# Kernel tuning notes

Measured on AMD Instinct MI355X. Metric: run time of the kernel, lower is better.

The kernel has to match this reference:

```python
import jax, jax.numpy as jnp
import numpy as np

N_PATCHES = 256
PATCH = 16
D = 768
H = 12
DH = D // H
L = 12
OUT_D = 10
EPS = 1e-5


def _pos_embed(seq_len, d):
    i = np.arange(seq_len)[:, None].astype(np.float64)
    j = np.arange(d)[None, :].astype(np.float64)
    angle_even = i / 10000 ** (j / d)
    angle_odd = i / 10000 ** ((j - 1) / d)
    pe = np.where(np.arange(d)[None, :] % 2 == 0, np.sin(angle_even), np.cos(angle_odd))
    return jnp.asarray(pe, dtype=jnp.float32)


def _layernorm(x, g, b):
    mu = jnp.mean(x, axis=-1, keepdims=True)
    var = jnp.var(x, axis=-1, keepdims=True)
    return (x - mu) * jax.lax.rsqrt(var + EPS) * g + b


def setup_inputs() -> dict:
    key = jax.random.key(0)
    ks = jax.random.split(key, 16)
    s = 0.02
    return {
        "images": jax.random.normal(ks[0], (64, 1, N_PATCHES * PATCH), dtype=jnp.float32),
        "Wemb": jax.random.normal(ks[1], (D, PATCH), dtype=jnp.float32) * s,
        "bemb": jnp.zeros((D,), jnp.float32),
        "cls": jax.random.uniform(ks[2], (1, D), dtype=jnp.float32),
        "Wq": jax.random.normal(ks[3], (L, H, DH, DH), dtype=jnp.float32) * s,
        "bq": jnp.zeros((L, H, DH), jnp.float32),
        "Wk": jax.random.normal(ks[4], (L, H, DH, DH), dtype=jnp.float32) * s,
        "bk": jnp.zeros((L, H, DH), jnp.float32),
        "Wv": jax.random.normal(ks[5], (L, H, DH, DH), dtype=jnp.float32) * s,
        "bv": jnp.zeros((L, H, DH), jnp.float32),
        "ln1_g": jnp.ones((L, D), jnp.float32),
        "ln1_b": jnp.zeros((L, D), jnp.float32),
        "ln2_g": jnp.ones((L, D), jnp.float32),
        "ln2_b": jnp.zeros((L, D), jnp.float32),
        "W1": jax.random.normal(ks[6], (L, 4 * D, D), dtype=jnp.float32) * s,
        "b1": jnp.zeros((L, 4 * D), jnp.float32),
        "W2": jax.random.normal(ks[7], (L, D, 4 * D), dtype=jnp.float32) * s,
        "b2": jnp.zeros((L, D), jnp.float32),
        "Whead": jax.random.normal(ks[8], (OUT_D, D), dtype=jnp.float32) * s,
        "bhead": jnp.zeros((OUT_D,), jnp.float32),
    }


def reference(images, Wemb, bemb, cls, Wq, bq, Wk, bk, Wv, bv,
              ln1_g, ln1_b, ln2_g, ln2_b, W1, b1, W2, b2, Whead, bhead):
    n = images.shape[0]
    # patchify: (N,1,Lspec) -> (N, n_patches, patch_size)
    patches = images.reshape(n, N_PATCHES, PATCH)
    tok = jnp.einsum("npi,di->npd", patches, Wemb) + bemb  # linear embed
    tok = jnp.concatenate([jnp.broadcast_to(cls[None], (n, 1, D)), tok], axis=1)
    tok = tok + _pos_embed(N_PATCHES + 1, D)[None]  # (N, S, D), S = 257

    scale = 1.0 / jnp.sqrt(jnp.float32(DH))
    for l in range(L):
        x = tok
        h = _layernorm(x, ln1_g[l], ln1_b[l]).reshape(n, -1, H, DH)
        q = jnp.einsum("nshd,hod->nsho", h, Wq[l]) + bq[l][None, None]
        k = jnp.einsum("nshd,hod->nsho", h, Wk[l]) + bk[l][None, None]
        v = jnp.einsum("nshd,hod->nsho", h, Wv[l]) + bv[l][None, None]
        att = jax.nn.softmax(jnp.einsum("nqho,nkho->nhqk", q, k) * scale, axis=-1)
        o = jnp.einsum("nhqk,nkho->nqho", att, v).reshape(n, -1, D)
        x = x + o  # residual (no output projection in original MSA)
        h2 = _layernorm(x, ln2_g[l], ln2_b[l])
        mlp = jax.nn.gelu(jnp.einsum("nsd,fd->nsf", h2, W1[l]) + b1[l], approximate=False)
        tok = x + jnp.einsum("nsf,df->nsd", mlp, W2[l]) + b2[l]

    logits = tok[:, 0] @ Whead.T + bhead
    return jax.nn.softmax(logits, axis=-1)
```

## Files before the change

### kernel.cpp

```cpp
#include <hip/hip_runtime.h>
#include <math.h>
#include <stdint.h>

#define N_IMG 64
#define S_LEN 257
#define D_MODEL 768
#define H_HEADS 12
#define L_LAYERS 12
#define F_HID 3072
#define OUT_DIM 10
#define R_ROWS (N_IMG * S_LEN)
#define R_PAD 16512
#define SKV 320

typedef unsigned short ushort_t;
typedef __attribute__((ext_vector_type(4))) float f32x4;
typedef __attribute__((ext_vector_type(8))) short short8;
typedef __attribute__((ext_vector_type(2))) unsigned int u32x2;

__device__ __forceinline__ ushort_t f2bf(float x) {
    unsigned u = __float_as_uint(x);
    u += 0x7fffu + ((u >> 16) & 1u);
    return (ushort_t)(u >> 16);
}
__device__ __forceinline__ unsigned pack2(float a, float b) {
    return (unsigned)f2bf(a) | ((unsigned)f2bf(b) << 16);
}

__device__ __forceinline__ void glds16(const ushort_t* g, const ushort_t* l) {
    __builtin_amdgcn_global_load_lds(
        (const __attribute__((address_space(1))) unsigned int*)(uintptr_t)g,
        (__attribute__((address_space(3))) unsigned int*)(uintptr_t)l,
        16, 0, 0);
}

__global__ __launch_bounds__(256) void pos_kernel(float* __restrict__ pos) {
    int i = blockIdx.x;
    int t = threadIdx.x;
    for (int u = 0; u < 3; ++u) {
        int j = t + 256 * u;
        double e = (double)(j & ~1) / 768.0;
        double angle = (double)i * exp(-e * 9.210340371976184);
        double v = (j & 1) ? cos(angle) : sin(angle);
        pos[i * 768 + j] = (float)v;
    }
}

__global__ __launch_bounds__(256) void embed_kernel(const float* __restrict__ images,
                                                    const float* __restrict__ Wemb,
                                                    const float* __restrict__ bemb,
                                                    const float* __restrict__ cls,
                                                    const float* __restrict__ pos,
                                                    float* __restrict__ tok) {
    int b = blockIdx.x;
    int n = b / S_LEN, s = b % S_LEN;
    int t = threadIdx.x;
    __shared__ float p[16];
    if (s > 0 && t < 16) p[t] = images[n * 4096 + (s - 1) * 16 + t];
    __syncthreads();
    for (int u = 0; u < 3; ++u) {
        int d = t + 256 * u;
        float acc;
        if (s == 0) {
            acc = cls[d];
        } else {
            acc = bemb[d];
            const float4* w = (const float4*)(Wemb + d * 16);
            float4 w0 = w[0], w1 = w[1], w2 = w[2], w3 = w[3];
            acc += p[0] * w0.x + p[1] * w0.y + p[2] * w0.z + p[3] * w0.w;
            acc += p[4] * w1.x + p[5] * w1.y + p[6] * w1.z + p[7] * w1.w;
            acc += p[8] * w2.x + p[9] * w2.y + p[10] * w2.z + p[11] * w2.w;
            acc += p[12] * w3.x + p[13] * w3.y + p[14] * w3.z + p[15] * w3.w;
        }
        tok[(size_t)b * 768 + d] = acc + pos[s * 768 + d];
    }
}

__global__ __launch_bounds__(256) void ln_kernel(const float* __restrict__ x,
                                                 const float* __restrict__ g,
                                                 const float* __restrict__ b,
                                                 ushort_t* __restrict__ y) {
    int row = blockIdx.x * 4 + (threadIdx.x >> 6);
    int lane = threadIdx.x & 63;
    const float* xr = x + (size_t)row * 768 + lane * 4;
    float4 a0 = *(const float4*)xr;
    float4 a1 = *(const float4*)(xr + 256);
    float4 a2 = *(const float4*)(xr + 512);
    float s = (a0.x + a0.y + a0.z + a0.w) + (a1.x + a1.y + a1.z + a1.w) + (a2.x + a2.y + a2.z + a2.w);
    float sq = a0.x*a0.x + a0.y*a0.y + a0.z*a0.z + a0.w*a0.w
             + a1.x*a1.x + a1.y*a1.y + a1.z*a1.z + a1.w*a1.w
             + a2.x*a2.x + a2.y*a2.y + a2.z*a2.z + a2.w*a2.w;
    for (int o = 32; o; o >>= 1) {
        s += __shfl_xor(s, o);
        sq += __shfl_xor(sq, o);
    }
    float mu = s * (1.0f / 768.0f);
    float var = sq * (1.0f / 768.0f) - mu * mu;
    float rs = rsqrtf(var + 1e-5f);
    ushort_t* yr = y + (size_t)row * 768 + lane * 4;
#pragma unroll
    for (int i = 0; i < 3; ++i) {
        float4 av = (i == 0) ? a0 : (i == 1) ? a1 : a2;
        const float4 gg = *(const float4*)(g + lane * 4 + i * 256);
        const float4 bb = *(const float4*)(b + lane * 4 + i * 256);
        float o0 = (av.x - mu) * rs * gg.x + bb.x;
        float o1 = (av.y - mu) * rs * gg.y + bb.y;
        float o2 = (av.z - mu) * rs * gg.z + bb.z;
        float o3 = (av.w - mu) * rs * gg.w + bb.w;
        *(u32x2*)(yr + i * 256) = (u32x2){pack2(o0, o1), pack2(o2, o3)};
    }
}

__global__ __launch_bounds__(256) void conv_layer(const float* __restrict__ Wq,
                                                  const float* __restrict__ Wk,
                                                  const float* __restrict__ Wv,
                                                  const float* __restrict__ W1l,
                                                  const float* __restrict__ W2l,
                                                  ushort_t* __restrict__ wqkvbf,
                                                  ushort_t* __restrict__ w1bf,
                                                  ushort_t* __restrict__ w2bf) {
    const int NQKV = H_HEADS * 192 * 64;
    const int NW = F_HID * D_MODEL;
    int idx = (blockIdx.x * 256 + threadIdx.x) * 4;
    if (idx < NQKV) {
        int h = idx / (192 * 64);
        int rem = idx - h * 192 * 64;
        int o3 = rem >> 6, d = rem & 63;
        const float* src;
        int o;
        if (o3 < 64)       { src = Wq; o = o3; }
        else if (o3 < 128) { src = Wk; o = o3 - 64; }
        else               { src = Wv; o = o3 - 128; }
        float4 v = *(const float4*)(src + ((size_t)(h * 64 + o)) * 64 + d);
        *(u32x2*)(wqkvbf + idx) = (u32x2){pack2(v.x, v.y), pack2(v.z, v.w)};
    } else if (idx < NQKV + NW) {
        int i = idx - NQKV;
        float4 v = *(const float4*)(W1l + i);
        *(u32x2*)(w1bf + i) = (u32x2){pack2(v.x, v.y), pack2(v.z, v.w)};
    } else {
        int i = idx - NQKV - NW;
        float4 v = *(const float4*)(W2l + i);
        *(u32x2*)(w2bf + i) = (u32x2){pack2(v.x, v.y), pack2(v.z, v.w)};
    }
}

__global__ __launch_bounds__(256) void qkv_mfma(const ushort_t* __restrict__ xbf,
                                                const ushort_t* __restrict__ wqkv,
                                                const float* __restrict__ bq,
                                                const float* __restrict__ bk,
                                                const float* __restrict__ bv,
                                                ushort_t* __restrict__ qhb,
                                                ushort_t* __restrict__ khb,
                                                ushort_t* __restrict__ vtb) {
    __shared__ ushort_t As[128 * 64];
    int rt = blockIdx.x;
    int h = blockIdx.y;
    int t = threadIdx.x, lane = t & 63, wid = t >> 6;
    int wr = wid >> 1, wc = wid & 1;
    {
        int lr = t >> 3, lg = t & 7;
#pragma unroll
        for (int u = 0; u < 4; ++u) {
            int r = u * 32 + lr;
            int grow = rt * 128 + r;
            if (grow >= R_ROWS) grow = R_ROWS - 1;
            short8 a = *(const short8*)(xbf + (size_t)grow * 768 + h * 64 + lg * 8);
            *(short8*)&As[r * 64 + (lg ^ (r & 7)) * 8] = a;
        }
    }
    __syncthreads();
    int frow = lane & 15, g = lane >> 4;
    const ushort_t* wb = wqkv + (size_t)h * (192 * 64);
    f32x4 acc[4][6];
#pragma unroll
    for (int m = 0; m < 4; ++m)
#pragma unroll
        for (int n = 0; n < 6; ++n) acc[m][n] = (f32x4){0.f, 0.f, 0.f, 0.f};
#pragma unroll
    for (int kk = 0; kk < 2; ++kk) {
        short8 af[4], bfr[6];
#pragma unroll
        for (int m = 0; m < 4; ++m) {
            int r = wr * 64 + m * 16 + frow;
            af[m] = *(const short8*)&As[r * 64 + ((kk * 4 + g) ^ (r & 7)) * 8];
        }
#pragma unroll
        for (int n = 0; n < 6; ++n)
            bfr[n] = *(const short8*)(wb + (size_t)(wc * 96 + n * 16 + frow) * 64 + kk * 32 + g * 8);
#pragma unroll
        for (int m = 0; m < 4; ++m)
#pragma unroll
            for (int n = 0; n < 6; ++n)
                acc[m][n] = __builtin_amdgcn_mfma_f32_16x16x32_bf16(bfr[n], af[m], acc[m][n], 0, 0, 0);
    }
#pragma unroll
    for (int m = 0; m < 4; ++m) {
        int token = rt * 128 + wr * 64 + m * 16 + frow;
        if (token < R_ROWS) {
            unsigned nimg = (unsigned)token / 257u;
            unsigned s = (unsigned)token - nimg * 257u;
            size_t qk_base = ((size_t)(nimg * H_HEADS + h) * 257 + s) * 64;
            size_t v_base = (size_t)(nimg * H_HEADS + h) * (64 * SKV);
#pragma unroll
            for (int n = 0; n < 6; ++n) {
                int c = wc * 96 + n * 16 + g * 4;
                f32x4 a = acc[m][n];
                if (c < 64) {
                    const float4 bb = *(const float4*)(bq + h * 64 + c);
                    *(u32x2*)(qhb + qk_base + c) = (u32x2){
                        pack2((a[0] + bb.x) * 0.125f, (a[1] + bb.y) * 0.125f),
                        pack2((a[2] + bb.z) * 0.125f, (a[3] + bb.w) * 0.125f)};
                } else if (c < 128) {
                    const float4 bb = *(const float4*)(bk + h * 64 + (c - 64));
                    *(u32x2*)(khb + qk_base + (c - 64)) = (u32x2){
                        pack2(a[0] + bb.x, a[1] + bb.y), pack2(a[2] + bb.z, a[3] + bb.w)};
                } else {
                    const float4 bb = *(const float4*)(bv + h * 64 + (c - 128));
                    vtb[v_base + (size_t)(c - 128 + 0) * SKV + s] = f2bf(a[0] + bb.x);
                    vtb[v_base + (size_t)(c - 128 + 1) * SKV + s] = f2bf(a[1] + bb.y);
                    vtb[v_base + (size_t)(c - 128 + 2) * SKV + s] = f2bf(a[2] + bb.z);
                    vtb[v_base + (size_t)(c - 128 + 3) * SKV + s] = f2bf(a[3] + bb.w);
                }
            }
        }
    }
}

template <int NST>
__global__ __launch_bounds__(256) void attn_mfma(const ushort_t* __restrict__ qh,
                                                 const ushort_t* __restrict__ kh,
                                                 const ushort_t* __restrict__ vT,
                                                 float* __restrict__ tok, int base) {
    __shared__ ushort_t Plds[4][NST][1024];
    int nh = blockIdx.x;
    int h = nh % H_HEADS, n = nh / H_HEADS;
    int t = threadIdx.x, w = t >> 6, lane = t & 63;
    int lq = lane & 15, g = lane >> 4;
    const size_t hoff = ((size_t)n * H_HEADS + h) * (S_LEN * 64);
    const ushort_t* qhp = qh + hoff;
    const ushort_t* khp = kh + hoff;
    const ushort_t* vp  = vT + ((size_t)n * H_HEADS + h) * (64 * SKV);
    const int xorm = (lq & 7) << 4;

    short8 qf[NST][2];
    int qr0[NST];
    float m[NST], lsum[NST];
    f32x4 o[NST][4];
#pragma unroll
    for (int s = 0; s < NST; ++s) {
        int qrow = base + s * 64 + w * 16 + lq;
        qr0[s] = qrow;
        int qcl = qrow > 256 ? 256 : qrow;
#pragma unroll
        for (int kk = 0; kk < 2; ++kk)
            qf[s][kk] = *(const short8*)(qhp + (size_t)qcl * 64 + kk * 32 + g * 8);
        m[s] = -INFINITY; lsum[s] = 0.f;
#pragma unroll
        for (int dt = 0; dt < 4; ++dt) o[s][dt] = (f32x4){0.f, 0.f, 0.f, 0.f};
    }

    for (int kt = 0; kt < 5; ++kt) {
        short8 ah[4][2];
#pragma unroll
        for (int st = 0; st < 4; ++st) {
            int key = kt * 64 + st * 16 + lq;
            int kcl = key > 256 ? 256 : key;
            const ushort_t* krh = khp + (size_t)kcl * 64 + g * 8;
            ah[st][0] = *(const short8*)krh;
            ah[st][1] = *(const short8*)(krh + 32);
        }
        f32x4 c[NST][4];
#pragma unroll
        for (int s = 0; s < NST; ++s)
#pragma unroll
            for (int st = 0; st < 4; ++st) {
                c[s][st] = (f32x4){0.f, 0.f, 0.f, 0.f};
#pragma unroll
                for (int kk = 0; kk < 2; ++kk)
                    c[s][st] = __builtin_amdgcn_mfma_f32_16x16x32_bf16(ah[st][kk], qf[s][kk], c[s][st], 0, 0, 0);
            }
        float scale[NST];
        unsigned pw[NST][4][2];
#pragma unroll
        for (int s = 0; s < NST; ++s) {
            float tmax = -INFINITY;
#pragma unroll
            for (int st = 0; st < 4; ++st)
#pragma unroll
                for (int j = 0; j < 4; ++j) {
                    int key = kt * 64 + st * 16 + g * 4 + j;
                    float sv = (key <= 256) ? c[s][st][j] : -INFINITY;
                    c[s][st][j] = sv;
                    tmax = fmaxf(tmax, sv);
                }
            tmax = fmaxf(tmax, __shfl_xor(tmax, 16));
            tmax = fmaxf(tmax, __shfl_xor(tmax, 32));
            float mn = fmaxf(m[s], tmax);
            scale[s] = __expf(m[s] - mn);
            float psum = 0.f;
#pragma unroll
            for (int st = 0; st < 4; ++st) {
                float p0 = __expf(c[s][st][0] - mn), p1 = __expf(c[s][st][1] - mn);
                float p2 = __expf(c[s][st][2] - mn), p3 = __expf(c[s][st][3] - mn);
                psum += (p0 + p1) + (p2 + p3);
                pw[s][st][0] = pack2(p0, p1);
                pw[s][st][1] = pack2(p2, p3);
            }
            psum += __shfl_xor(psum, 16);
            psum += __shfl_xor(psum, 32);
            lsum[s] = lsum[s] * scale[s] + psum;
            m[s] = mn;
        }
#pragma unroll
        for (int s = 0; s < NST; ++s) {
            char* pwave = (char*)&Plds[w][s][0];
#pragma unroll
            for (int st = 0; st < 4; ++st) {
                int off = (lq * 128 + st * 32 + g * 8) ^ xorm;
                *(u32x2*)(pwave + off) = (u32x2){pw[s][st][0], pw[s][st][1]};
            }
#pragma unroll
            for (int dt = 0; dt < 4; ++dt) {
                o[s][dt][0] *= scale[s]; o[s][dt][1] *= scale[s];
                o[s][dt][2] *= scale[s]; o[s][dt][3] *= scale[s];
            }
        }
#pragma unroll
        for (int kk = 0; kk < 2; ++kk) {
            short8 pf[NST];
#pragma unroll
            for (int s = 0; s < NST; ++s) {
                int roff = (lq * 128 + kk * 64 + g * 16) ^ xorm;
                pf[s] = *(const short8*)((char*)&Plds[w][s][0] + roff);
            }
#pragma unroll
            for (int dt = 0; dt < 4; ++dt) {
                short8 vf = *(const short8*)(vp + (size_t)(dt * 16 + lq) * SKV + kt * 64 + kk * 32 + g * 8);
#pragma unroll
                for (int s = 0; s < NST; ++s)
                    o[s][dt] = __builtin_amdgcn_mfma_f32_16x16x32_bf16(vf, pf[s], o[s][dt], 0, 0, 0);
            }
        }
    }
#pragma unroll
    for (int s = 0; s < NST; ++s) {
        if (qr0[s] < S_LEN) {
            float inv = 1.0f / lsum[s];
            float* trow = tok + ((size_t)n * S_LEN + qr0[s]) * 768 + h * 64 + g * 4;
#pragma unroll
            for (int dt = 0; dt < 4; ++dt) {
                float4 old = *(const float4*)(trow + dt * 16);
                old.x += o[s][dt][0] * inv;
                old.y += o[s][dt][1] * inv;
                old.z += o[s][dt][2] * inv;
                old.w += o[s][dt][3] * inv;
                *(float4*)(trow + dt * 16) = old;
            }
        }
    }
}

__device__ __forceinline__ float gelu_fast(float x) {
    float s = fabsf(x) * 0.70710678118654752f;
    float t = 1.0f / (1.0f + 0.3275911f * s);
    float y = t * (0.254829592f + t * (-0.284496736f + t * (1.421413741f +
              t * (-1.453152027f + t * 1.061405429f))));
    float erfa = 1.0f - y * __expf(-s * s);
    float erfv = copysignf(erfa, x);
    return 0.5f * x * (1.0f + erfv);
}

template <int MODE>
__global__ __launch_bounds__(256) void mfma_gemm(const ushort_t* __restrict__ A,
                                                 const ushort_t* __restrict__ B,
                                                 const float* __restrict__ bias,
                                                 void* __restrict__ Cv,
                                                 int K, int lda, int ldb, int ldc, int nbn) {
    __shared__ ushort_t As[2][128 * 64];
    __shared__ ushort_t Bs[2][128 * 64];
    int nwg = gridDim.x;
    int orig = blockIdx.x;
    int xcd = orig & 7, idx = orig >> 3;
    int q8 = nwg >> 3, r8 = nwg & 7;
    int cbase = (xcd < r8) ? xcd * (q8 + 1) : r8 * (q8 + 1) + (xcd - r8) * q8;
    int swz = cbase + idx;
    int bm = swz / nbn, bn = swz - bm * nbn;

    int t = threadIdx.x;
    int lane = t & 63, wid = t >> 6;
    int wr = wid >> 1, wc = wid & 1;
    const ushort_t* Ag = A + (size_t)(bm * 128) * lda;
    const ushort_t* Bg = B + (size_t)(bn * 128) * ldb;
    int srow = t >> 3;
    int swzo = ((t & 7) ^ (srow & 7)) * 8;
    int wbase = (t & 192) * 8;
    int frow = lane & 15, g = lane >> 4;
    f32x4 acc[4][4];
#pragma unroll
    for (int m = 0; m < 4; ++m)
#pragma unroll
        for (int n = 0; n < 4; ++n) acc[m][n] = (f32x4){0.f, 0.f, 0.f, 0.f};

    auto STAGE = [&](int buf, int k0) {
#pragma unroll
        for (int u = 0; u < 4; ++u) {
            glds16(Ag + (size_t)(u * 32 + srow) * lda + k0 + swzo, &As[buf][u * 2048 + wbase]);
            glds16(Bg + (size_t)(u * 32 + srow) * ldb + k0 + swzo, &Bs[buf][u * 2048 + wbase]);
        }
    };
    STAGE(0, 0);
    asm volatile("s_waitcnt vmcnt(0)" ::: "memory");
    __builtin_amdgcn_s_barrier();
    int nt = K >> 6;
    int cur = 0;
    for (int it = 0; it < nt; ++it) {
        if (it + 1 < nt) STAGE(cur ^ 1, (it + 1) * 64);
        const ushort_t* Ab = &As[cur][0];
        const ushort_t* Bb = &Bs[cur][0];
#pragma unroll
        for (int kk = 0; kk < 2; ++kk) {
            short8 af[4], bfr[4];
#pragma unroll
            for (int mi = 0; mi < 4; ++mi) {
                int r = wr * 64 + mi * 16 + frow;
                af[mi] = *(const short8*)&Ab[r * 64 + ((kk * 4 + g) ^ (r & 7)) * 8];
            }
#pragma unroll
            for (int ni = 0; ni < 4; ++ni) {
                int r = wc * 64 + ni * 16 + frow;
                bfr[ni] = *(const short8*)&Bb[r * 64 + ((kk * 4 + g) ^ (r & 7)) * 8];
            }
#pragma unroll
            for (int mi = 0; mi < 4; ++mi)
#pragma unroll
                for (int ni = 0; ni < 4; ++ni)
                    acc[mi][ni] = __builtin_amdgcn_mfma_f32_16x16x32_bf16(bfr[ni], af[mi], acc[mi][ni], 0, 0, 0);
        }
        if (it + 1 < nt) {
            asm volatile("s_waitcnt vmcnt(0) lgkmcnt(0)" ::: "memory");
            __builtin_amdgcn_s_barrier();
            cur ^= 1;
        }
    }
    int row0 = bm * 128 + wr * 64 + frow;
    int col0 = bn * 128 + wc * 64 + g * 4;
#pragma unroll
    for (int n = 0; n < 4; ++n) {
        int col = col0 + n * 16;
        float4 bb = {0.f, 0.f, 0.f, 0.f};
        if (bias) bb = *(const float4*)(bias + col);
#pragma unroll
        for (int mi = 0; mi < 4; ++mi) {
            int row = row0 + mi * 16;
            f32x4 a = acc[mi][n];
            float v0 = a[0] + bb.x, v1 = a[1] + bb.y, v2 = a[2] + bb.z, v3 = a[3] + bb.w;
            if (MODE == 0) {
                v0 = gelu_fast(v0); v1 = gelu_fast(v1); v2 = gelu_fast(v2); v3 = gelu_fast(v3);
                *(u32x2*)((ushort_t*)Cv + (size_t)row * ldc + col) =
                    (u32x2){pack2(v0, v1), pack2(v2, v3)};
            } else {
                float* cp = (float*)Cv + (size_t)row * ldc + col;
                float4 old = *(const float4*)cp;
                old.x += v0; old.y += v1; old.z += v2; old.w += v3;
                *(float4*)cp = old;
            }
        }
    }
}

__global__ __launch_bounds__(64) void head_kernel(const float* __restrict__ tok,
                                                  const float* __restrict__ Whead,
                                                  const float* __restrict__ bhead,
                                                  float* __restrict__ out) {
    int n = blockIdx.x;
    int t = threadIdx.x;
    __shared__ float logits[OUT_DIM];
    if (t < OUT_DIM) {
        float acc = bhead[t];
        const float* xr = tok + (size_t)n * S_LEN * 768;
        const float* w = Whead + t * 768;
        for (int d = 0; d < 768; ++d) acc += xr[d] * w[d];
        logits[t] = acc;
    }
    __syncthreads();
    if (t == 0) {
        float m = -INFINITY;
        for (int o = 0; o < OUT_DIM; ++o) m = fmaxf(m, logits[o]);
        float ssum = 0.f;
        float e[OUT_DIM];
        for (int o = 0; o < OUT_DIM; ++o) { e[o] = expf(logits[o] - m); ssum += e[o]; }
        float inv = 1.0f / ssum;
        for (int o = 0; o < OUT_DIM; ++o) out[n * OUT_DIM + o] = e[o] * inv;
    }
}

extern "C" void kernel_launch(void* const* d_in, const int* in_sizes, int n_in,
                              void* d_out, int out_size, void* d_ws, size_t ws_size,
                              hipStream_t stream) {
    const float* images = (const float*)d_in[0];
    const float* Wemb   = (const float*)d_in[1];
    const float* bemb   = (const float*)d_in[2];
    const float* cls    = (const float*)d_in[3];
    const float* Wq     = (const float*)d_in[4];
    const float* bq     = (const float*)d_in[5];
    const float* Wk     = (const float*)d_in[6];
    const float* bk     = (const float*)d_in[7];
    const float* Wv     = (const float*)d_in[8];
    const float* bv     = (const float*)d_in[9];
    const float* ln1_g  = (const float*)d_in[10];
    const float* ln1_b  = (const float*)d_in[11];
    const float* ln2_g  = (const float*)d_in[12];
    const float* ln2_b  = (const float*)d_in[13];
    const float* W1     = (const float*)d_in[14];
    const float* b1     = (const float*)d_in[15];
    const float* W2     = (const float*)d_in[16];
    const float* b2     = (const float*)d_in[17];
    const float* Whead  = (const float*)d_in[18];
    const float* bhead  = (const float*)d_in[19];
    float* out = (float*)d_out;

    const size_t TOKP = (size_t)R_PAD * D_MODEL;
    const size_t QKSZ = (size_t)N_IMG * H_HEADS * S_LEN * 64;
    const size_t VTSZ = (size_t)N_IMG * H_HEADS * 64 * SKV;
    const size_t WSZ  = (size_t)F_HID * D_MODEL;
    float* ws   = (float*)d_ws;
    float* pos  = ws;
    float* tok  = pos + 197376;
    ushort_t* xbf  = (ushort_t*)(tok + TOKP);
    ushort_t* qhb  = xbf + TOKP;
    ushort_t* khb  = qhb + QKSZ;
    ushort_t* vtb  = khb + QKSZ;
    ushort_t* wqkvbf = vtb + VTSZ;
    ushort_t* w1bf = wqkvbf + H_HEADS * 192 * 64;
    ushort_t* w2bf = w1bf + WSZ;
    ushort_t* hid_full = w2bf + WSZ;

    const size_t hid_bytes = (size_t)R_PAD * F_HID * 2;
    const size_t needed = ((char*)hid_full - (char*)d_ws) + hid_bytes;
    int nchunk = (ws_size >= needed) ? 1 : 2;
    int FC = F_HID / nchunk;
    ushort_t* hid = (nchunk == 1) ? hid_full : qhb;

    pos_kernel<<<S_LEN, 256, 0, stream>>>(pos);
    embed_kernel<<<R_ROWS, 256, 0, stream>>>(images, Wemb, bemb, cls, pos, tok);

    for (int l = 0; l < L_LAYERS; ++l) {
        const size_t wqkv_off = (size_t)l * H_HEADS * 64 * 64;
        const size_t bqkv_off = (size_t)l * H_HEADS * 64;
        ln_kernel<<<R_ROWS / 4, 256, 0, stream>>>(tok, ln1_g + l * 768, ln1_b + l * 768, xbf);
        conv_layer<<<4752, 256, 0, stream>>>(
            Wq + wqkv_off, Wk + wqkv_off, Wv + wqkv_off,
            W1 + (size_t)l * WSZ, W2 + (size_t)l * WSZ,
            wqkvbf, w1bf, w2bf);
        qkv_mfma<<<dim3(R_PAD / 128, H_HEADS), 256, 0, stream>>>(
            xbf, wqkvbf, bq + bqkv_off, bk + bqkv_off, bv + bqkv_off, qhb, khb, vtb);
        attn_mfma<2><<<N_IMG * H_HEADS, 256, 0, stream>>>(qhb, khb, vtb, tok, 0);
        attn_mfma<3><<<N_IMG * H_HEADS, 256, 0, stream>>>(qhb, khb, vtb, tok, 128);
        ln_kernel<<<R_ROWS / 4, 256, 0, stream>>>(tok, ln2_g + l * 768, ln2_b + l * 768, xbf);
        for (int c = 0; c < nchunk; ++c) {
            int c0 = c * FC;
            mfma_gemm<0><<<(FC / 128) * (R_PAD / 128), 256, 0, stream>>>(
                xbf, w1bf + (size_t)c0 * D_MODEL, b1 + (size_t)l * F_HID + c0, hid,
                768, 768, 768, FC, FC / 128);
            mfma_gemm<1><<<(D_MODEL / 128) * (R_PAD / 128), 256, 0, stream>>>(
                hid, w2bf + c0, (c == 0) ? (b2 + (size_t)l * D_MODEL) : (const float*)nullptr,
                tok, FC, FC, F_HID, D_MODEL, D_MODEL / 128);
        }
    }
    head_kernel<<<N_IMG, 64, 0, stream>>>(tok, Whead, bhead, out);
}
```

Measured before the change: 4.823 ms.

## Enlarge MLP GEMM tiles to 256x256 with 512 threads and 4-stage LDS pipeline

Rewrites the MLP GEMM kernel to use 256x256 output tiles across 8 waves, with a K-step of 32 and a four-buffer global-to-LDS prefetch ring driven by vmcnt-based waits. Row padding grows so row counts divide by 256, and the QKV launch keeps its old grid size. The larger tiles are meant to raise arithmetic intensity and hide load latency better. In exchange, register pressure rises (32 accumulator tiles per wave), the grid has fewer blocks, which may leave CUs idle (the W2 GEMM gets only 3 column tiles), and there is extra padded work.

```diff
diff --git a/kernel.cpp b/kernel.cpp
--- a/kernel.cpp
+++ b/kernel.cpp
@@ -10,7 +10,7 @@
 #define F_HID 3072
 #define OUT_DIM 10
 #define R_ROWS (N_IMG * S_LEN)
-#define R_PAD 16512
+#define R_PAD 16640
 #define SKV 320
 
 typedef unsigned short ushort_t;
@@ -371,13 +371,13 @@
 }
 
 template <int MODE>
-__global__ __launch_bounds__(256) void mfma_gemm(const ushort_t* __restrict__ A,
-                                                 const ushort_t* __restrict__ B,
-                                                 const float* __restrict__ bias,
-                                                 void* __restrict__ Cv,
-                                                 int K, int lda, int ldb, int ldc, int nbn) {
-    __shared__ ushort_t As[2][128 * 64];
-    __shared__ ushort_t Bs[2][128 * 64];
+__global__ __launch_bounds__(512, 2) void mfma_gemm(const ushort_t* __restrict__ A,
+                                                    const ushort_t* __restrict__ B,
+                                                    const float* __restrict__ bias,
+                                                    void* __restrict__ Cv,
+                                                    int K, int lda, int ldb, int ldc, int nbn) {
+    __shared__ ushort_t As[4][256 * 32];
+    __shared__ ushort_t Bs[4][256 * 32];
     int nwg = gridDim.x;
     int orig = blockIdx.x;
     int xcd = orig & 7, idx = orig >> 3;
@@ -387,72 +387,71 @@
     int bm = swz / nbn, bn = swz - bm * nbn;
 
     int t = threadIdx.x;
-    int lane = t & 63, wid = t >> 6;
-    int wr = wid >> 1, wc = wid & 1;
-    const ushort_t* Ag = A + (size_t)(bm * 128) * lda;
-    const ushort_t* Bg = B + (size_t)(bn * 128) * ldb;
-    int srow = t >> 3;
-    int swzo = ((t & 7) ^ (srow & 7)) * 8;
-    int wbase = (t & 192) * 8;
+    int lane = t & 63, w = t >> 6;
+    int wr = w >> 2, wc = w & 3;
+    const ushort_t* Ag = A + (size_t)(bm * 256) * lda;
+    const ushort_t* Bg = B + (size_t)(bn * 256) * ldb;
     int frow = lane & 15, g = lane >> 4;
-    f32x4 acc[4][4];
-#pragma unroll
-    for (int m = 0; m < 4; ++m)
+    int srow = lane >> 2;
+    int scol = ((lane & 3) ^ ((lane >> 3) & 3)) * 8;
+    int rslot = (frow >> 1) & 3;
+
+    f32x4 acc[8][4];
+#pragma unroll
+    for (int m = 0; m < 8; ++m)
 #pragma unroll
         for (int n = 0; n < 4; ++n) acc[m][n] = (f32x4){0.f, 0.f, 0.f, 0.f};
 
-    auto STAGE = [&](int buf, int k0) {
-#pragma unroll
-        for (int u = 0; u < 4; ++u) {
-            glds16(Ag + (size_t)(u * 32 + srow) * lda + k0 + swzo, &As[buf][u * 2048 + wbase]);
-            glds16(Bg + (size_t)(u * 32 + srow) * ldb + k0 + swzo, &Bs[buf][u * 2048 + wbase]);
+    auto STAGE = [&](int buf, int kt) {
+        int k0 = kt * 32;
+#pragma unroll
+        for (int i = 0; i < 2; ++i) {
+            int rbase = w * 32 + i * 16;
+            glds16(Ag + (size_t)(rbase + srow) * lda + k0 + scol, &As[buf][rbase * 32]);
+            glds16(Bg + (size_t)(rbase + srow) * ldb + k0 + scol, &Bs[buf][rbase * 32]);
         }
     };
     STAGE(0, 0);
-    asm volatile("s_waitcnt vmcnt(0)" ::: "memory");
-    __builtin_amdgcn_s_barrier();
-    int nt = K >> 6;
-    int cur = 0;
+    STAGE(1, 1);
+    STAGE(2, 2);
+    int nt = K >> 5;
     for (int it = 0; it < nt; ++it) {
-        if (it + 1 < nt) STAGE(cur ^ 1, (it + 1) * 64);
-        const ushort_t* Ab = &As[cur][0];
-        const ushort_t* Bb = &Bs[cur][0];
-#pragma unroll
-        for (int kk = 0; kk < 2; ++kk) {
-            short8 af[4], bfr[4];
-#pragma unroll
-            for (int mi = 0; mi < 4; ++mi) {
-                int r = wr * 64 + mi * 16 + frow;
-                af[mi] = *(const short8*)&Ab[r * 64 + ((kk * 4 + g) ^ (r & 7)) * 8];
-            }
-#pragma unroll
-            for (int ni = 0; ni < 4; ++ni) {
-                int r = wc * 64 + ni * 16 + frow;
-                bfr[ni] = *(const short8*)&Bb[r * 64 + ((kk * 4 + g) ^ (r & 7)) * 8];
-            }
-#pragma unroll
-            for (int mi = 0; mi < 4; ++mi)
-#pragma unroll
-                for (int ni = 0; ni < 4; ++ni)
-                    acc[mi][ni] = __builtin_amdgcn_mfma_f32_16x16x32_bf16(bfr[ni], af[mi], acc[mi][ni], 0, 0, 0);
-        }
-        if (it + 1 < nt) {
-            asm volatile("s_waitcnt vmcnt(0) lgkmcnt(0)" ::: "memory");
-            __builtin_amdgcn_s_barrier();
-            cur ^= 1;
-        }
-    }
-    int row0 = bm * 128 + wr * 64 + frow;
-    int col0 = bn * 128 + wc * 64 + g * 4;
+        int ahead = nt - 1 - it;
+        if (ahead >= 2)      asm volatile("s_waitcnt vmcnt(8)" ::: "memory");
+        else if (ahead == 1) asm volatile("s_waitcnt vmcnt(4)" ::: "memory");
+        else                 asm volatile("s_waitcnt vmcnt(0)" ::: "memory");
+        asm volatile("s_barrier" ::: "memory");
+        if (it + 3 < nt) STAGE((it + 3) & 3, it + 3);
+        const ushort_t* Ab = &As[it & 3][0];
+        const ushort_t* Bb = &Bs[it & 3][0];
+        short8 af[8], bf[4];
+#pragma unroll
+        for (int m = 0; m < 8; ++m) {
+            int r = wr * 128 + m * 16 + frow;
+            af[m] = *(const short8*)&Ab[r * 32 + ((g ^ rslot) * 8)];
+        }
+#pragma unroll
+        for (int n = 0; n < 4; ++n) {
+            int r = wc * 64 + n * 16 + frow;
+            bf[n] = *(const short8*)&Bb[r * 32 + ((g ^ rslot) * 8)];
+        }
+#pragma unroll
+        for (int m = 0; m < 8; ++m)
+#pragma unroll
+            for (int n = 0; n < 4; ++n)
+                acc[m][n] = __builtin_amdgcn_mfma_f32_16x16x32_bf16(bf[n], af[m], acc[m][n], 0, 0, 0);
+    }
+    int row0 = bm * 256 + wr * 128 + frow;
+    int col0 = bn * 256 + wc * 64 + g * 4;
 #pragma unroll
     for (int n = 0; n < 4; ++n) {
         int col = col0 + n * 16;
         float4 bb = {0.f, 0.f, 0.f, 0.f};
         if (bias) bb = *(const float4*)(bias + col);
 #pragma unroll
-        for (int mi = 0; mi < 4; ++mi) {
-            int row = row0 + mi * 16;
-            f32x4 a = acc[mi][n];
+        for (int m = 0; m < 8; ++m) {
+            int row = row0 + m * 16;
+            f32x4 a = acc[m][n];
             float v0 = a[0] + bb.x, v1 = a[1] + bb.y, v2 = a[2] + bb.z, v3 = a[3] + bb.w;
             if (MODE == 0) {
                 v0 = gelu_fast(v0); v1 = gelu_fast(v1); v2 = gelu_fast(v2); v3 = gelu_fast(v3);
@@ -552,19 +551,19 @@
             Wq + wqkv_off, Wk + wqkv_off, Wv + wqkv_off,
             W1 + (size_t)l * WSZ, W2 + (size_t)l * WSZ,
             wqkvbf, w1bf, w2bf);
-        qkv_mfma<<<dim3(R_PAD / 128, H_HEADS), 256, 0, stream>>>(
+        qkv_mfma<<<dim3(16512 / 128, H_HEADS), 256, 0, stream>>>(
             xbf, wqkvbf, bq + bqkv_off, bk + bqkv_off, bv + bqkv_off, qhb, khb, vtb);
         attn_mfma<2><<<N_IMG * H_HEADS, 256, 0, stream>>>(qhb, khb, vtb, tok, 0);
         attn_mfma<3><<<N_IMG * H_HEADS, 256, 0, stream>>>(qhb, khb, vtb, tok, 128);
         ln_kernel<<<R_ROWS / 4, 256, 0, stream>>>(tok, ln2_g + l * 768, ln2_b + l * 768, xbf);
         for (int c = 0; c < nchunk; ++c) {
             int c0 = c * FC;
-            mfma_gemm<0><<<(FC / 128) * (R_PAD / 128), 256, 0, stream>>>(
+            mfma_gemm<0><<<(FC / 256) * (R_PAD / 256), 512, 0, stream>>>(
                 xbf, w1bf + (size_t)c0 * D_MODEL, b1 + (size_t)l * F_HID + c0, hid,
-                768, 768, 768, FC, FC / 128);
-            mfma_gemm<1><<<(D_MODEL / 128) * (R_PAD / 128), 256, 0, stream>>>(
+                768, 768, 768, FC, FC / 256);
+            mfma_gemm<1><<<(D_MODEL / 256) * (R_PAD / 256), 512, 0, stream>>>(
                 hid, w2bf + c0, (c == 0) ? (b2 + (size_t)l * D_MODEL) : (const float*)nullptr,
-                tok, FC, FC, F_HID, D_MODEL, D_MODEL / 128);
+                tok, FC, FC, F_HID, D_MODEL, D_MODEL / 256);
         }
     }
     head_kernel<<<N_IMG, 64, 0, stream>>>(tok, Whead, bhead, out);
```

Result: slower. 5.060 ms (+4.9%).

## Load GEMM B operand directly from global and fuse attention launches

Applied to the files above, without the earlier changes.

The MLP GEMM no longer stages the weight (B) tile through LDS. Each wave loads its B fragments straight from global memory into registers, which halves shared memory use, and launch bounds request four blocks per CU to raise occupancy. The two attention kernel launches, covering the two query ranges, are merged into a single launch with a doubled grid that branches on block parity. In exchange, B loads lose LDS reuse and double-buffered prefetch and depend on cache hits, and the occupancy hint may cause register spilling.

```diff
diff --git a/kernel.cpp b/kernel.cpp
--- a/kernel.cpp
+++ b/kernel.cpp
@@ -227,20 +227,16 @@
 }
 
 template <int NST>
-__global__ __launch_bounds__(256) void attn_mfma(const ushort_t* __restrict__ qh,
-                                                 const ushort_t* __restrict__ kh,
-                                                 const ushort_t* __restrict__ vT,
-                                                 float* __restrict__ tok, int base) {
-    __shared__ ushort_t Plds[4][NST][1024];
-    int nh = blockIdx.x;
-    int h = nh % H_HEADS, n = nh / H_HEADS;
-    int t = threadIdx.x, w = t >> 6, lane = t & 63;
+__device__ __forceinline__ void attn_body(ushort_t* Pl,
+                                          const ushort_t* __restrict__ qhp,
+                                          const ushort_t* __restrict__ khp,
+                                          const ushort_t* __restrict__ vp,
+                                          float* __restrict__ tok,
+                                          int n, int h, int base, int t) {
+    int w = t >> 6, lane = t & 63;
     int lq = lane & 15, g = lane >> 4;
-    const size_t hoff = ((size_t)n * H_HEADS + h) * (S_LEN * 64);
-    const ushort_t* qhp = qh + hoff;
-    const ushort_t* khp = kh + hoff;
-    const ushort_t* vp  = vT + ((size_t)n * H_HEADS + h) * (64 * SKV);
     const int xorm = (lq & 7) << 4;
+    char* pw0 = (char*)(Pl + (size_t)w * 3 * 1024);
 
     short8 qf[NST][2];
     int qr0[NST];
@@ -313,7 +309,7 @@
         }
 #pragma unroll
         for (int s = 0; s < NST; ++s) {
-            char* pwave = (char*)&Plds[w][s][0];
+            char* pwave = pw0 + s * 2048;
 #pragma unroll
             for (int st = 0; st < 4; ++st) {
                 int off = (lq * 128 + st * 32 + g * 8) ^ xorm;
@@ -331,7 +327,7 @@
 #pragma unroll
             for (int s = 0; s < NST; ++s) {
                 int roff = (lq * 128 + kk * 64 + g * 16) ^ xorm;
-                pf[s] = *(const short8*)((char*)&Plds[w][s][0] + roff);
+                pf[s] = *(const short8*)(pw0 + s * 2048 + roff);
             }
 #pragma unroll
             for (int dt = 0; dt < 4; ++dt) {
@@ -358,6 +354,24 @@
             }
         }
     }
+}
+
+__global__ __launch_bounds__(256) void attn_fused(const ushort_t* __restrict__ qh,
+                                                  const ushort_t* __restrict__ kh,
+                                                  const ushort_t* __restrict__ vT,
+                                                  float* __restrict__ tok) {
+    __shared__ ushort_t Plds[4 * 3 * 1024];
+    int b = blockIdx.x;
+    int half = b & 1;
+    int nh = b >> 1;
+    int h = nh % H_HEADS, n = nh / H_HEADS;
+    const size_t hoff = ((size_t)n * H_HEADS + h) * (S_LEN * 64);
+    const ushort_t* qhp = qh + hoff;
+    const ushort_t* khp = kh + hoff;
+    const ushort_t* vp  = vT + ((size_t)n * H_HEADS + h) * (64 * SKV);
+    int t = threadIdx.x;
+    if (half == 0) attn_body<2>(Plds, qhp, khp, vp, tok, n, h, 0, t);
+    else           attn_body<3>(Plds, qhp, khp, vp, tok, n, h, 128, t);
 }
 
 __device__ __forceinline__ float gelu_fast(float x) {
@@ -371,30 +385,34 @@
 }
 
 template <int MODE>
-__global__ __launch_bounds__(256) void mfma_gemm(const ushort_t* __restrict__ A,
-                                                 const ushort_t* __restrict__ B,
-                                                 const float* __restrict__ bias,
-                                                 void* __restrict__ Cv,
-                                                 int K, int lda, int ldb, int ldc, int nbn) {
+__global__ __launch_bounds__(256, 4) void mfma_gemm(const ushort_t* __restrict__ A,
+                                                    const ushort_t* __restrict__ B,
+                                                    const float* __restrict__ bias,
+                                                    void* __restrict__ Cv,
+                                                    int K, int lda, int ldb, int ldc, int nbn) {
     __shared__ ushort_t As[2][128 * 64];
-    __shared__ ushort_t Bs[2][128 * 64];
     int nwg = gridDim.x;
     int orig = blockIdx.x;
     int xcd = orig & 7, idx = orig >> 3;
     int q8 = nwg >> 3, r8 = nwg & 7;
     int cbase = (xcd < r8) ? xcd * (q8 + 1) : r8 * (q8 + 1) + (xcd - r8) * q8;
-    int swz = cbase + idx;
-    int bm = swz / nbn, bn = swz - bm * nbn;
+    int swb = cbase + idx;
+    int bm = swb / nbn, bn = swb - bm * nbn;
 
     int t = threadIdx.x;
     int lane = t & 63, wid = t >> 6;
     int wr = wid >> 1, wc = wid & 1;
     const ushort_t* Ag = A + (size_t)(bm * 128) * lda;
-    const ushort_t* Bg = B + (size_t)(bn * 128) * ldb;
     int srow = t >> 3;
     int swzo = ((t & 7) ^ (srow & 7)) * 8;
     int wbase = (t & 192) * 8;
     int frow = lane & 15, g = lane >> 4;
+
+    const ushort_t* bp[4];
+#pragma unroll
+    for (int n = 0; n < 4; ++n)
+        bp[n] = B + (size_t)(bn * 128 + wc * 64 + n * 16 + frow) * ldb + g * 8;
+
     f32x4 acc[4][4];
 #pragma unroll
     for (int m = 0; m < 4; ++m)
@@ -403,10 +421,8 @@
 
     auto STAGE = [&](int buf, int k0) {
 #pragma unroll
-        for (int u = 0; u < 4; ++u) {
+        for (int u = 0; u < 4; ++u)
             glds16(Ag + (size_t)(u * 32 + srow) * lda + k0 + swzo, &As[buf][u * 2048 + wbase]);
-            glds16(Bg + (size_t)(u * 32 + srow) * ldb + k0 + swzo, &Bs[buf][u * 2048 + wbase]);
-        }
     };
     STAGE(0, 0);
     asm volatile("s_waitcnt vmcnt(0)" ::: "memory");
@@ -414,21 +430,19 @@
     int nt = K >> 6;
     int cur = 0;
     for (int it = 0; it < nt; ++it) {
-        if (it + 1 < nt) STAGE(cur ^ 1, (it + 1) * 64);
+        int k0 = it * 64;
+        if (it + 1 < nt) STAGE(cur ^ 1, k0 + 64);
         const ushort_t* Ab = &As[cur][0];
-        const ushort_t* Bb = &Bs[cur][0];
 #pragma unroll
         for (int kk = 0; kk < 2; ++kk) {
             short8 af[4], bfr[4];
+#pragma unroll
+            for (int ni = 0; ni < 4; ++ni)
+                bfr[ni] = *(const short8*)(bp[ni] + k0 + kk * 32);
 #pragma unroll
             for (int mi = 0; mi < 4; ++mi) {
                 int r = wr * 64 + mi * 16 + frow;
                 af[mi] = *(const short8*)&Ab[r * 64 + ((kk * 4 + g) ^ (r & 7)) * 8];
-            }
-#pragma unroll
-            for (int ni = 0; ni < 4; ++ni) {
-                int r = wc * 64 + ni * 16 + frow;
-                bfr[ni] = *(const short8*)&Bb[r * 64 + ((kk * 4 + g) ^ (r & 7)) * 8];
             }
 #pragma unroll
             for (int mi = 0; mi < 4; ++mi)
@@ -554,8 +568,7 @@
             wqkvbf, w1bf, w2bf);
         qkv_mfma<<<dim3(R_PAD / 128, H_HEADS), 256, 0, stream>>>(
             xbf, wqkvbf, bq + bqkv_off, bk + bqkv_off, bv + bqkv_off, qhb, khb, vtb);
-        attn_mfma<2><<<N_IMG * H_HEADS, 256, 0, stream>>>(qhb, khb, vtb, tok, 0);
-        attn_mfma<3><<<N_IMG * H_HEADS, 256, 0, stream>>>(qhb, khb, vtb, tok, 128);
+        attn_fused<<<N_IMG * H_HEADS * 2, 256, 0, stream>>>(qhb, khb, vtb, tok);
         ln_kernel<<<R_ROWS / 4, 256, 0, stream>>>(tok, ln2_g + l * 768, ln2_b + l * 768, xbf);
         for (int c = 0; c < nchunk; ++c) {
             int c0 = c * FC;
```

Result: slower. 6.912 ms (+43.3%).
